# Optimization experiments

Measured on AMD Instinct MI355X. Metric: run time of the kernel, lower is better.

## Reference

```python
import jax, jax.numpy as jnp
import numpy as np

TAU = 2.0
EPS_COH = 1e-8
EPS_NLL = 1e-7
ALPHA = 0.0
# component-vs-modality mask: rows = (common, synergy, g_spec, p_spec), cols = (gene, path)
MASK = np.array([[1.0, 1.0], [0.0, 0.0], [1.0, 0.0], [0.0, 1.0]], dtype=np.float32)


def l2norm(x, axis=-1):
    n = jnp.sqrt(jnp.sum(x * x, axis=axis, keepdims=True))
    return x / jnp.maximum(n, 1e-12)


def setup_inputs() -> dict:
    key = jax.random.key(0)
    ks = jax.random.split(key, 8)
    B, K, C, N = 64, 4, 256, 8192
    hazards = jax.random.uniform(ks[0], (B, K), dtype=jnp.float32)
    S = jnp.cumprod(1.0 - hazards, axis=1)  # survival curve, matches torch semantics
    indiv = jax.random.normal(ks[1], (B, 4, C), dtype=jnp.float32)
    gene = jax.random.normal(ks[2], (B, 1, C), dtype=jnp.float32)
    path = jax.random.normal(ks[3], (B, 1, C), dtype=jnp.float32)
    cohort_bank = jax.random.normal(ks[4], (K, N, 4, C), dtype=jnp.float32)
    label = jax.random.randint(ks[5], (B,), 0, K).astype(jnp.int32)
    c = jax.random.randint(ks[6], (B,), 0, 2).astype(jnp.int32)
    return {"hazards": hazards, "S": S, "indiv": indiv, "gene": gene,
            "path": path, "cohort_bank": cohort_bank, "label": label, "c": c}


def reference(hazards, S, indiv, gene, path, cohort_bank, label, c):
    B, K = hazards.shape
    dt = hazards.dtype
    # ---- NLLSurvLoss ----
    cf = c.astype(dt)[:, None]                       # [B,1] censoring flag
    Y = label.astype(jnp.int32)[:, None]             # [B,1]
    S_padded = jnp.concatenate([jnp.ones((B, 1), dt), S], axis=1)  # [B,K+1]
    s_y = jnp.take_along_axis(S_padded, Y, axis=1)
    h_y = jnp.take_along_axis(hazards, Y, axis=1)
    s_y1 = jnp.take_along_axis(S_padded, Y + 1, axis=1)
    clamp = lambda x: jnp.maximum(x, EPS_NLL)
    uncensored = -(1.0 - cf) * (jnp.log(clamp(s_y)) + jnp.log(clamp(h_y)))
    censored = -cf * jnp.log(clamp(s_y1))
    neg_l = censored + uncensored
    nll = ((1.0 - ALPHA) * neg_l + ALPHA * uncensored).mean()
    # ---- CohortLoss: intra ----
    indiv_n = l2norm(indiv)                          # [B,4,C]
    gp_n = l2norm(jnp.concatenate([gene, path], axis=1))  # [B,2,C]
    sim = jnp.einsum('bpc,btc->bpt', indiv_n, gp_n)  # [B,4,2]
    mask = jnp.asarray(MASK, dtype=dt)               # [4,2]
    intra = (jnp.abs(sim) * (1.0 - mask) - mask * sim).mean(axis=(1, 2)) + 1.0
    intra_loss = intra.mean()
    # ---- CohortLoss: inter (vectorized cohort-bank retrieval) ----
    n_cls, N = cohort_bank.shape[0], cohort_bank.shape[1]
    anchors = l2norm(indiv.mean(axis=1))             # [B,C]
    bank_means = cohort_bank.mean(axis=2)            # [n_cls,N,C]
    bank_n = l2norm(bank_means)                      # [n_cls,N,C]
    sims = jnp.einsum('knc,bc->bkn', bank_n, anchors)  # [B,n_cls,N]
    e = jnp.exp(sims / TAU)
    pos_mask = (label[:, None] == jnp.arange(n_cls, dtype=label.dtype)[None, :]).astype(dt)[:, :, None]  # [B,n_cls,1]
    ep = jnp.sum(e * pos_mask) / (B * N)                       # mean over B*N positive sims
    en = jnp.sum(e * (1.0 - pos_mask)) / (B * (n_cls - 1) * N)  # mean over B*(n_cls-1)*N negative sims
    inter_loss = -jnp.log((ep + EPS_COH) / (ep + en + EPS_COH))
    cohort_loss = intra_loss + inter_loss
    # Loss_factory: total = 1.0*nllsurv + 1.0*cohort
    return nll + cohort_loss
```

## Files before the change

kernel.cpp:

```cpp
#include <hip/hip_runtime.h>
#include <math.h>

#define BB 64
#define KK 4
#define CC 256
#define NN 8192
#define NROWS (KK*NN)
#define GRID_INTER 512
#define WPG 8
#define RPW 8
#define RPP 4
#define NPASS (RPW/RPP)

#define WS_A2_OFF    0
#define WS_SLOT_OFF  65536
#define WS_NLL_OFF   73728
#define WS_INTRA_OFF 73984
#define WS_TKT_OFF   74240

#define EPS_NLL 1e-7f

__device__ __forceinline__ float4 f4add(float4 a, float4 b){ return make_float4(a.x+b.x, a.y+b.y, a.z+b.z, a.w+b.w); }
__device__ __forceinline__ float4 f4scale(float4 a, float s){ return make_float4(a.x*s, a.y*s, a.z*s, a.w*s); }
__device__ __forceinline__ float dot4(float4 a, float4 b){ return a.x*b.x + a.y*b.y + a.z*b.z + a.w*b.w; }

__device__ __forceinline__ float wred(float v){
#pragma unroll
  for (int m = 32; m >= 1; m >>= 1) v += __shfl_xor(v, m, 64);
  return v;
}

__device__ __forceinline__ float rl(float v, int l){
  return __uint_as_float(__builtin_amdgcn_readlane(__float_as_uint(v), l));
}

__global__ __launch_bounds__(64) void prep_kernel(
    const float* __restrict__ hazards, const float* __restrict__ S,
    const float* __restrict__ indiv,   const float* __restrict__ gene,
    const float* __restrict__ path,    const int* __restrict__ label,
    const int* __restrict__ cvec,      char* __restrict__ ws)
{
  const int b = blockIdx.x;
  const int lane = threadIdx.x;

  const float4* ind4 = (const float4*)indiv + (size_t)b * 256;
  float4 i0 = ind4[  0 + lane];
  float4 i1 = ind4[ 64 + lane];
  float4 i2 = ind4[128 + lane];
  float4 i3 = ind4[192 + lane];
  float4 g  = ((const float4*)gene)[b*64 + lane];
  float4 p  = ((const float4*)path)[b*64 + lane];

  float4 am = f4scale(f4add(f4add(i0, i1), f4add(i2, i3)), 0.25f);
  float na = sqrtf(wred(dot4(am, am)));
  float4 an = f4scale(am, 1.0f / fmaxf(na, 1e-12f));
  ((float4*)(ws + WS_A2_OFF))[lane*64 + b] = an;

  float4 v[6] = {i0, i1, i2, i3, g, p};
#pragma unroll
  for (int j = 0; j < 6; ++j) {
    float n = sqrtf(wred(dot4(v[j], v[j])));
    v[j] = f4scale(v[j], 1.0f / fmaxf(n, 1e-12f));
  }

  float s[4][2];
#pragma unroll
  for (int pp = 0; pp < 4; ++pp)
#pragma unroll
    for (int t = 0; t < 2; ++t)
      s[pp][t] = wred(dot4(v[pp], v[4+t]));

  if (lane == 0) {
    float intra = (-s[0][0]) + (-s[0][1])
                + fabsf(s[1][0]) + fabsf(s[1][1])
                + (-s[2][0]) + fabsf(s[2][1])
                + fabsf(s[3][0]) + (-s[3][1]);
    intra = intra * 0.125f + 1.0f;
    ((float*)(ws + WS_INTRA_OFF))[b] = intra;

    int   Y  = label[b];
    float cf = (float)cvec[b];
    float s_y  = (Y == 0) ? 1.0f : S[b*KK + Y - 1];
    float s_y1 = S[b*KK + Y];
    float h_y  = hazards[b*KK + Y];
    float neg_l = -cf * logf(fmaxf(s_y1, EPS_NLL))
                  - (1.0f - cf) * (logf(fmaxf(s_y, EPS_NLL)) + logf(fmaxf(h_y, EPS_NLL)));
    ((float*)(ws + WS_NLL_OFF))[b] = neg_l;
  }
}

__global__ __launch_bounds__(512, 4) void inter_kernel(
    const float* __restrict__ bank, const int* __restrict__ label,
    char* __restrict__ ws, float* __restrict__ out)
{
  __shared__ float4 A2s[4096];
  __shared__ double redw[WPG][2];
  __shared__ unsigned tkt_s;

  const int tid  = threadIdx.x;
  const int wave = tid >> 6;
  const int lane = tid & 63;

  const float4* A2g = (const float4*)(ws + WS_A2_OFF);
#pragma unroll
  for (int i = 0; i < 8; ++i) A2s[tid + i*512] = A2g[tid + i*512];
  __syncthreads();

  const int myLab = label[lane];
  const int gw    = blockIdx.x * WPG + wave;
  const int base  = gw * RPW;
  const int kk    = base >> 13;
  const bool ispos = (myLab == kk);
  const float4* bank4 = (const float4*)bank;

  float accE = 0.0f;

#pragma unroll 1
  for (int pass = 0; pass < NPASS; ++pass) {
    const int row0 = base + pass * RPP;

    float4 m[RPP];
#pragma unroll
    for (int r = 0; r < RPP; ++r) {
      const float4* rp = bank4 + (size_t)(row0 + r) * 256 + lane;
      float4 a0 = rp[0], a1 = rp[64], a2 = rp[128], a3 = rp[192];
      m[r] = f4scale(f4add(f4add(a0, a1), f4add(a2, a3)), 0.25f);
    }
#pragma unroll
    for (int r = 0; r < RPP; ++r) {
      float n = sqrtf(wred(dot4(m[r], m[r])));
      m[r] = f4scale(m[r], 1.0f / fmaxf(n, 1e-12f));
    }

    float s0 = 0.0f, s1 = 0.0f, s2 = 0.0f, s3 = 0.0f;
#pragma unroll 4
    for (int cq = 0; cq < 64; ++cq) {
      float4 a = A2s[cq*64 + lane];
      s0 += a.x*rl(m[0].x,cq) + a.y*rl(m[0].y,cq) + a.z*rl(m[0].z,cq) + a.w*rl(m[0].w,cq);
      s1 += a.x*rl(m[1].x,cq) + a.y*rl(m[1].y,cq) + a.z*rl(m[1].z,cq) + a.w*rl(m[1].w,cq);
      s2 += a.x*rl(m[2].x,cq) + a.y*rl(m[2].y,cq) + a.z*rl(m[2].z,cq) + a.w*rl(m[2].w,cq);
      s3 += a.x*rl(m[3].x,cq) + a.y*rl(m[3].y,cq) + a.z*rl(m[3].z,cq) + a.w*rl(m[3].w,cq);
    }

    accE += expf(s0 * 0.5f) + expf(s1 * 0.5f)
          + expf(s2 * 0.5f) + expf(s3 * 0.5f);
  }

  float epf = ispos ? accE : 0.0f;
  float enf = ispos ? 0.0f : accE;
  epf = wred(epf);
  enf = wred(enf);
  if (lane == 0) {
    redw[wave][0] = (double)epf;
    redw[wave][1] = (double)enf;
  }
  __syncthreads();

  double*   slots  = (double*)(ws + WS_SLOT_OFF);
  unsigned* ticket = (unsigned*)(ws + WS_TKT_OFF);

  if (tid == 0) {
    double bep = 0.0, ben = 0.0;
#pragma unroll
    for (int w = 0; w < WPG; ++w) { bep += redw[w][0]; ben += redw[w][1]; }
    slots[blockIdx.x*2 + 0] = bep;
    slots[blockIdx.x*2 + 1] = ben;
    __threadfence();
    tkt_s = atomicAdd(ticket, 1u);
  }
  __syncthreads();

  if (tkt_s == GRID_INTER - 1 && wave == 0) {
    __threadfence();
    double pep = 0.0, pen = 0.0;
    for (int i = lane; i < GRID_INTER; i += 64) {
      pep += slots[2*i + 0];
      pen += slots[2*i + 1];
    }
#pragma unroll
    for (int m = 32; m >= 1; m >>= 1) {
      pep += __shfl_xor(pep, m, 64);
      pen += __shfl_xor(pen, m, 64);
    }
    float scal = ((const float*)(ws + WS_NLL_OFF))[lane]
               + ((const float*)(ws + WS_INTRA_OFF))[lane];
    scal = wred(scal);
    if (lane == 0) {
      double ep = pep / (double)(BB * NN);
      double en = pen / (double)(BB * (KK-1) * NN);
      double inter = -log((ep + 1e-8) / (ep + en + 1e-8));
      out[0] = (float)((double)scal / 64.0 + inter);
    }
  }
}

extern "C" void kernel_launch(void* const* d_in, const int* in_sizes, int n_in,
                              void* d_out, int out_size, void* d_ws, size_t ws_size,
                              hipStream_t stream)
{
  const float* hazards = (const float*)d_in[0];
  const float* S       = (const float*)d_in[1];
  const float* indiv   = (const float*)d_in[2];
  const float* gene    = (const float*)d_in[3];
  const float* path    = (const float*)d_in[4];
  const float* bank    = (const float*)d_in[5];
  const int*   label   = (const int*)d_in[6];
  const int*   cvec    = (const int*)d_in[7];
  char*  ws  = (char*)d_ws;
  float* out = (float*)d_out;

  hipMemsetAsync(ws + WS_TKT_OFF, 0, 4, stream);
  prep_kernel<<<dim3(BB), dim3(64), 0, stream>>>(hazards, S, indiv, gene, path, label, cvec, ws);
  inter_kernel<<<dim3(GRID_INTER), dim3(512), 0, stream>>>(bank, label, ws, out);
}
```

Baseline: 233.8 us.

## Compute bank-anchor similarities with bf16 MFMA instead of scalar readlane dot products

Replaces the per-row readlane-broadcast FP32 dot-product loop with 16x16x32 bf16 MFMA tiles. The prep kernel now writes the normalized anchors to the workspace as bf16, pre-swizzled into the MFMA B-operand layout. Each wave loads 16 bank rows, averages and normalizes them in registers, converts them to bf16 and multiplies them against all 64 anchors. The block shrinks to 4 waves. This removes the VALU/readlane-bound inner loop, at the cost of bf16 rounding of the similarities before the exp.

```diff
diff --git a/kernel.cpp b/kernel.cpp
--- a/kernel.cpp
+++ b/kernel.cpp
@@ -7,18 +7,19 @@
 #define NN 8192
 #define NROWS (KK*NN)
 #define GRID_INTER 512
-#define WPG 8
-#define RPW 8
-#define RPP 4
-#define NPASS (RPW/RPP)
-
-#define WS_A2_OFF    0
-#define WS_SLOT_OFF  65536
-#define WS_NLL_OFF   73728
-#define WS_INTRA_OFF 73984
-#define WS_TKT_OFF   74240
+#define WPG 4
+#define TILES (GRID_INTER*WPG)
+
+#define WS_B_OFF     0
+#define WS_SLOT_OFF  32768
+#define WS_NLL_OFF   40960
+#define WS_INTRA_OFF 41216
+#define WS_TKT_OFF   41472
 
 #define EPS_NLL 1e-7f
+
+typedef __attribute__((ext_vector_type(8))) short bf16x8;
+typedef __attribute__((ext_vector_type(4))) float f32x4;
 
 __device__ __forceinline__ float4 f4add(float4 a, float4 b){ return make_float4(a.x+b.x, a.y+b.y, a.z+b.z, a.w+b.w); }
 __device__ __forceinline__ float4 f4scale(float4 a, float s){ return make_float4(a.x*s, a.y*s, a.z*s, a.w*s); }
@@ -30,8 +31,10 @@
   return v;
 }
 
-__device__ __forceinline__ float rl(float v, int l){
-  return __uint_as_float(__builtin_amdgcn_readlane(__float_as_uint(v), l));
+__device__ __forceinline__ unsigned short f2bf(float x){
+  union { float f; unsigned u; } v; v.f = x;
+  unsigned r = v.u + 0x7fffu + ((v.u >> 16) & 1u);
+  return (unsigned short)(r >> 16);
 }
 
 __global__ __launch_bounds__(64) void prep_kernel(
@@ -54,7 +57,17 @@
   float4 am = f4scale(f4add(f4add(i0, i1), f4add(i2, i3)), 0.25f);
   float na = sqrtf(wred(dot4(am, am)));
   float4 an = f4scale(am, 1.0f / fmaxf(na, 1e-12f));
-  ((float4*)(ws + WS_A2_OFF))[lane*64 + b] = an;
+
+  {
+    const int cq = lane;
+    const unsigned addr = (unsigned)((cq >> 3) * 4096
+                        + (b >> 4) * 1024
+                        + ((((cq >> 1) & 3) * 16) + (b & 15)) * 16
+                        + (cq & 1) * 8);
+    ushort4 h4;
+    h4.x = f2bf(an.x); h4.y = f2bf(an.y); h4.z = f2bf(an.z); h4.w = f2bf(an.w);
+    *(ushort4*)(ws + WS_B_OFF + addr) = h4;
+  }
 
   float4 v[6] = {i0, i1, i2, i3, g, p};
 #pragma unroll
@@ -89,65 +102,86 @@
   }
 }
 
-__global__ __launch_bounds__(512, 4) void inter_kernel(
+__global__ __launch_bounds__(256) void inter_kernel(
     const float* __restrict__ bank, const int* __restrict__ label,
     char* __restrict__ ws, float* __restrict__ out)
 {
-  __shared__ float4 A2s[4096];
+  __shared__ uint4 Bl[2048];
   __shared__ double redw[WPG][2];
   __shared__ unsigned tkt_s;
 
   const int tid  = threadIdx.x;
   const int wave = tid >> 6;
   const int lane = tid & 63;
-
-  const float4* A2g = (const float4*)(ws + WS_A2_OFF);
-#pragma unroll
-  for (int i = 0; i < 8; ++i) A2s[tid + i*512] = A2g[tid + i*512];
+  const int lm   = lane & 15;
+  const int lg   = lane >> 4;
+
+  const uint4* Bg = (const uint4*)(ws + WS_B_OFF);
+#pragma unroll
+  for (int i = 0; i < 8; ++i) Bl[tid + i*256] = Bg[tid + i*256];
   __syncthreads();
 
-  const int myLab = label[lane];
-  const int gw    = blockIdx.x * WPG + wave;
-  const int base  = gw * RPW;
-  const int kk    = base >> 13;
-  const bool ispos = (myLab == kk);
-  const float4* bank4 = (const float4*)bank;
-
-  float accE = 0.0f;
-
-#pragma unroll 1
-  for (int pass = 0; pass < NPASS; ++pass) {
-    const int row0 = base + pass * RPP;
-
-    float4 m[RPP];
-#pragma unroll
-    for (int r = 0; r < RPP; ++r) {
-      const float4* rp = bank4 + (size_t)(row0 + r) * 256 + lane;
-      float4 a0 = rp[0], a1 = rp[64], a2 = rp[128], a3 = rp[192];
-      m[r] = f4scale(f4add(f4add(a0, a1), f4add(a2, a3)), 0.25f);
-    }
-#pragma unroll
-    for (int r = 0; r < RPP; ++r) {
-      float n = sqrtf(wred(dot4(m[r], m[r])));
-      m[r] = f4scale(m[r], 1.0f / fmaxf(n, 1e-12f));
-    }
-
-    float s0 = 0.0f, s1 = 0.0f, s2 = 0.0f, s3 = 0.0f;
-#pragma unroll 4
-    for (int cq = 0; cq < 64; ++cq) {
-      float4 a = A2s[cq*64 + lane];
-      s0 += a.x*rl(m[0].x,cq) + a.y*rl(m[0].y,cq) + a.z*rl(m[0].z,cq) + a.w*rl(m[0].w,cq);
-      s1 += a.x*rl(m[1].x,cq) + a.y*rl(m[1].y,cq) + a.z*rl(m[1].z,cq) + a.w*rl(m[1].w,cq);
-      s2 += a.x*rl(m[2].x,cq) + a.y*rl(m[2].y,cq) + a.z*rl(m[2].z,cq) + a.w*rl(m[2].w,cq);
-      s3 += a.x*rl(m[3].x,cq) + a.y*rl(m[3].y,cq) + a.z*rl(m[3].z,cq) + a.w*rl(m[3].w,cq);
-    }
-
-    accE += expf(s0 * 0.5f) + expf(s1 * 0.5f)
-          + expf(s2 * 0.5f) + expf(s3 * 0.5f);
-  }
-
-  float epf = ispos ? accE : 0.0f;
-  float enf = ispos ? 0.0f : accE;
+  const int gw   = blockIdx.x * WPG + wave;
+  const int row0 = gw * 16;
+  const int kk   = row0 >> 13;
+
+  int lab[4];
+#pragma unroll
+  for (int nt = 0; nt < 4; ++nt) lab[nt] = label[nt*16 + lm];
+
+  const float* rp = bank + (size_t)(row0 + lm) * 1024 + lg * 8;
+
+  float4 sA[8][2];
+#pragma unroll
+  for (int kc = 0; kc < 8; ++kc)
+#pragma unroll
+    for (int p = 0; p < 2; ++p)
+      sA[kc][p] = *(const float4*)(rp + kc*32 + p*4);
+#pragma unroll
+  for (int c = 1; c < 4; ++c)
+#pragma unroll
+    for (int kc = 0; kc < 8; ++kc)
+#pragma unroll
+      for (int p = 0; p < 2; ++p) {
+        float4 t = *(const float4*)(rp + c*256 + kc*32 + p*4);
+        sA[kc][p] = f4add(sA[kc][p], t);
+      }
+
+  float ss = 0.0f;
+#pragma unroll
+  for (int kc = 0; kc < 8; ++kc)
+#pragma unroll
+    for (int p = 0; p < 2; ++p)
+      ss += dot4(sA[kc][p], sA[kc][p]);
+  ss += __shfl_xor(ss, 16, 64);
+  ss += __shfl_xor(ss, 32, 64);
+  const float rs = rsqrtf(fmaxf(ss, 1e-24f));
+
+  f32x4 acc0 = {0,0,0,0}, acc1 = {0,0,0,0}, acc2 = {0,0,0,0}, acc3 = {0,0,0,0};
+#pragma unroll
+  for (int kc = 0; kc < 8; ++kc) {
+    float4 u = sA[kc][0], v = sA[kc][1];
+    bf16x8 a;
+    a[0] = (short)f2bf(u.x*rs); a[1] = (short)f2bf(u.y*rs);
+    a[2] = (short)f2bf(u.z*rs); a[3] = (short)f2bf(u.w*rs);
+    a[4] = (short)f2bf(v.x*rs); a[5] = (short)f2bf(v.y*rs);
+    a[6] = (short)f2bf(v.z*rs); a[7] = (short)f2bf(v.w*rs);
+    acc0 = __builtin_amdgcn_mfma_f32_16x16x32_bf16(a, *(const bf16x8*)&Bl[(kc*4+0)*64 + lane], acc0, 0, 0, 0);
+    acc1 = __builtin_amdgcn_mfma_f32_16x16x32_bf16(a, *(const bf16x8*)&Bl[(kc*4+1)*64 + lane], acc1, 0, 0, 0);
+    acc2 = __builtin_amdgcn_mfma_f32_16x16x32_bf16(a, *(const bf16x8*)&Bl[(kc*4+2)*64 + lane], acc2, 0, 0, 0);
+    acc3 = __builtin_amdgcn_mfma_f32_16x16x32_bf16(a, *(const bf16x8*)&Bl[(kc*4+3)*64 + lane], acc3, 0, 0, 0);
+  }
+
+  float epf = 0.0f, enf = 0.0f;
+#define DO_NT(ACC, NT)                                                        \
+  {                                                                           \
+    float es = expf(ACC.x * 0.5f) + expf(ACC.y * 0.5f)                        \
+             + expf(ACC.z * 0.5f) + expf(ACC.w * 0.5f);                       \
+    if (lab[NT] == kk) epf += es; else enf += es;                             \
+  }
+  DO_NT(acc0, 0) DO_NT(acc1, 1) DO_NT(acc2, 2) DO_NT(acc3, 3)
+#undef DO_NT
+
   epf = wred(epf);
   enf = wred(enf);
   if (lane == 0) {
@@ -211,5 +245,5 @@
 
   hipMemsetAsync(ws + WS_TKT_OFF, 0, 4, stream);
   prep_kernel<<<dim3(BB), dim3(64), 0, stream>>>(hazards, S, indiv, gene, path, label, cvec, ws);
-  inter_kernel<<<dim3(GRID_INTER), dim3(512), 0, stream>>>(bank, label, ws, out);
-}
+  inter_kernel<<<dim3(GRID_INTER), dim3(256), 0, stream>>>(bank, label, ws, out);
+}
```

Result: no change. 235.3 us (+0.6%).
